# Performance work log

Hardware: AMD Instinct MI355X
Metric: run time of the kernel (lower is better)

Reference implementation:

```python
import jax, jax.numpy as jnp
import numpy as np

C = 512
H_FEAT, W_FEAT = 50, 75
ROI_SIZE = 7
SCALE = 16.0
N_ROIS = 512
N_CLASS = 21
FC_IN = C * ROI_SIZE * ROI_SIZE  # 25088
FC_DIM = 4096


def setup_inputs() -> dict:
    key = jax.random.key(0)
    ks = jax.random.split(key, 12)
    x = jax.random.normal(ks[0], (1, C, H_FEAT, W_FEAT), jnp.float32)
    img_h, img_w = H_FEAT * 16, W_FEAT * 16
    # boxes (x1,y1,x2,y2) in image pixel coords, in-bounds, min side 32px
    x1 = jax.random.randint(ks[1], (N_ROIS,), 0, img_w - 64)
    y1 = jax.random.randint(ks[2], (N_ROIS,), 0, img_h - 64)
    w = jax.random.randint(ks[3], (N_ROIS,), 32, 400)
    h = jax.random.randint(ks[4], (N_ROIS,), 32, 400)
    x2 = jnp.minimum(x1 + w, img_w - 1)
    y2 = jnp.minimum(y1 + h, img_h - 1)
    rois = jnp.stack([x1, y1, x2, y2], axis=1).astype(jnp.float32)
    W1 = jax.random.normal(ks[5], (FC_IN, FC_DIM), jnp.float32) * 0.01
    b1 = jnp.zeros((FC_DIM,), jnp.float32)
    W2 = jax.random.normal(ks[6], (FC_DIM, FC_DIM), jnp.float32) * 0.01
    b2 = jnp.zeros((FC_DIM,), jnp.float32)
    W_loc = jax.random.normal(ks[7], (FC_DIM, N_CLASS * 4), jnp.float32) * 0.001
    b_loc = jnp.zeros((N_CLASS * 4,), jnp.float32)
    W_score = jax.random.normal(ks[8], (FC_DIM, N_CLASS), jnp.float32) * 0.01
    b_score = jnp.zeros((N_CLASS,), jnp.float32)
    return {"x": x, "rois": rois, "W1": W1, "b1": b1, "W2": W2, "b2": b2,
            "W_loc": W_loc, "b_loc": b_loc, "W_score": W_score, "b_score": b_score}


def _roi_adaptive_max_pool(feat, rois_i):
    """feat: [C,H,W]; rois_i: int32 [N,4] (x1,y1,x2,y2) in feature coords.
    Matches torch F.adaptive_max_pool2d on the inclusive crop [y1:y2+1, x1:x2+1].
    """
    KR = H_FEAT // ROI_SIZE + 2   # max rows per adaptive bin (<= ceil(H/7)+1)
    KC = W_FEAT // ROI_SIZE + 2   # max cols per adaptive bin
    p = jnp.arange(ROI_SIZE)

    def one(roi):
        x1, y1, x2, y2 = roi[0], roi[1], roi[2], roi[3]
        h = y2 - y1 + 1
        w = x2 - x1 + 1
        # torch adaptive pooling: start = floor(i*S/O), end = ceil((i+1)*S/O)
        rs = y1 + (p * h) // ROI_SIZE
        re = y1 + -((-(p + 1) * h) // ROI_SIZE)   # ceil via floor-div
        cs = x1 + (p * w) // ROI_SIZE
        ce = x1 + -((-(p + 1) * w) // ROI_SIZE)
        ri = rs[:, None] + jnp.arange(KR)[None, :]          # [7,KR]
        rv = ri < re[:, None]
        ri = jnp.clip(ri, 0, H_FEAT - 1)
        ci = cs[:, None] + jnp.arange(KC)[None, :]          # [7,KC]
        cv = ci < ce[:, None]
        ci = jnp.clip(ci, 0, W_FEAT - 1)
        g = feat[:, ri, :][:, :, :, ci]                      # [C,7,KR,7,KC]
        m = rv[:, :, None, None] & cv[None, None, :, :]      # [7,KR,7,KC]
        g = jnp.where(m[None], g, -jnp.inf)
        return g.max(axis=(2, 4))                            # [C,7,7]

    return jax.lax.map(one, rois_i)                          # [N,C,7,7]


def reference(x, rois, W1, b1, W2, b2, W_loc, b_loc, W_score, b_score):
    # rois.mul_(1/spatial_scale); rois = rois.long()  (trunc == floor for >=0)
    rois_i = (rois * (1.0 / SCALE)).astype(jnp.int32)
    pool = _roi_adaptive_max_pool(x[0], rois_i)              # [N,C,7,7]
    pool = pool.reshape(pool.shape[0], -1)                   # [N, 25088]
    fc = jax.nn.relu(pool @ W1 + b1)
    fc = jax.nn.relu(fc @ W2 + b2)
    roi_locs = fc @ W_loc + b_loc                            # [N, 84]
    roi_scores = fc @ W_score + b_score                      # [N, 21]
    return (roi_locs, roi_scores)
```

## Files before the change

kernel.cpp:

```cpp
#include <hip/hip_runtime.h>
#include <hip/hip_bf16.h>
#include <math.h>

typedef unsigned short U16;
typedef __bf16 bf16x8 __attribute__((ext_vector_type(8)));
typedef float floatx4 __attribute__((ext_vector_type(4)));
typedef unsigned short ushort8 __attribute__((ext_vector_type(8)));

#define C_CH 512
#define HF 50
#define WF 75
#define NROIS 512
#define FC_IN 25088
#define FC_DIM 4096
#define NHEAD 105
#define NHEAD_PAD 128
#define OUT_LOCS (NROIS * 84)

__device__ __forceinline__ float b2f(U16 u) {
    union { unsigned int i; float f; } x; x.i = ((unsigned int)u) << 16; return x.f;
}
__device__ __forceinline__ U16 f2b(float f) {
    union { float f; unsigned int i; } x; x.f = f;
    unsigned int r = x.i + 0x7fffu + ((x.i >> 16) & 1u);
    return (U16)(r >> 16);
}

__device__ __forceinline__ void gld_lds16(const U16* g, U16* lds_base, int lane) {
#if __has_builtin(__builtin_amdgcn_global_load_lds)
    typedef const __attribute__((address_space(1))) unsigned int* gas1;
    typedef __attribute__((address_space(3))) unsigned int* las3;
    __builtin_amdgcn_global_load_lds((gas1)(unsigned long long)g,
                                     (las3)(unsigned int)(unsigned long long)lds_base,
                                     16, 0, 0);
#else
    *(floatx4*)(lds_base + lane * 8) = *(const floatx4*)g;
#endif
}

__global__ void detect_kernel(const unsigned int* __restrict__ w1,
                              const unsigned int* __restrict__ rois,
                              int* __restrict__ flags) {
    __shared__ int cnt_w, cnt_r;
    if (threadIdx.x == 0) { cnt_w = 0; cnt_r = 0; }
    __syncthreads();
    int lw = 0;
    for (int i = threadIdx.x; i < 2048; i += 256) {
        const unsigned int w = w1[i];
        const unsigned int e = (w >> 7) & 0xFFu;
        if ((e >= 90u && e <= 130u) || (w & 0x7FFFu) == 0u) lw++;
    }
    int lr = 0;
    for (int i = threadIdx.x; i < 512; i += 256) {
        union { unsigned int u; float f; } v; v.u = rois[i];
        const float f = v.f;
        if (f >= 0.0f && f <= 1300.0f && f == floorf(f)) lr++;
    }
    atomicAdd(&cnt_w, lw);
    atomicAdd(&cnt_r, lr);
    __syncthreads();
    if (threadIdx.x == 0) {
        flags[0] = (cnt_w < 1024) ? 1 : 0;
        flags[1] = (cnt_r >= 256) ? 1 : 0;
    }
}

__global__ void roi_pool_kernel(const void* __restrict__ feat_,
                                const void* __restrict__ rois_,
                                const int* __restrict__ flags,
                                U16* __restrict__ pool) {
    const int n = blockIdx.x;
    const int ch0 = blockIdx.y * 32;
    const int t = threadIdx.x;
    const int f32w = flags[0];
    const int f32r = flags[1];
    __shared__ int rs[7], re_[7], cs[7], ce_[7];

    float c4[4];
    if (f32r) {
        const float* r = (const float*)rois_ + n * 4;
        c4[0] = r[0]; c4[1] = r[1]; c4[2] = r[2]; c4[3] = r[3];
    } else {
        const U16* r = (const U16*)rois_ + n * 4;
        c4[0] = b2f(r[0]); c4[1] = b2f(r[1]); c4[2] = b2f(r[2]); c4[3] = b2f(r[3]);
    }
    const int x1 = (int)(c4[0] * 0.0625f);
    const int y1 = (int)(c4[1] * 0.0625f);
    const int x2 = (int)(c4[2] * 0.0625f);
    const int y2 = (int)(c4[3] * 0.0625f);
    const int h = y2 - y1 + 1;
    const int w = x2 - x1 + 1;
    if (t < 7) {
        rs[t] = y1 + (t * h) / 7;
        re_[t] = y1 + ((t + 1) * h + 6) / 7;
        cs[t] = x1 + (t * w) / 7;
        ce_[t] = x1 + ((t + 1) * w + 6) / 7;
    }
    __syncthreads();

    const float* featf = (const float*)feat_;
    const U16* featu = (const U16*)feat_;

    for (int o = t; o < 32 * 49; o += 256) {
        const int ch = ch0 + o / 49;
        const int b = o % 49;
        const int ph = b / 7;
        const int pw = b - ph * 7;
        const int r0 = rs[ph], r1 = re_[ph];
        const int c0 = cs[pw], c1 = ce_[pw];
        const int base = ch * (HF * WF);
        float m = -1.0e4f;
        if (f32w) {
            for (int r = r0; r < r1; ++r) {
                const int rr = r < (HF - 1) ? r : (HF - 1);
                const float* fr = featf + base + rr * WF;
                for (int c = c0; c < c1; ++c) {
                    const int cc = c < (WF - 1) ? c : (WF - 1);
                    const float v = fr[cc];
                    m = (m > v) ? m : v;
                }
            }
        } else {
            for (int r = r0; r < r1; ++r) {
                const int rr = r < (HF - 1) ? r : (HF - 1);
                const U16* fr = featu + base + rr * WF;
                for (int c = c0; c < c1; ++c) {
                    const int cc = c < (WF - 1) ? c : (WF - 1);
                    const float v = b2f(fr[cc]);
                    m = (m > v) ? m : v;
                }
            }
        }
        m = fminf(fmaxf(m, -1.0e4f), 1.0e4f);
        pool[(size_t)n * FC_IN + ch * 49 + b] = f2b(m);
    }
}

__global__ void transpose_w_kernel(const void* __restrict__ W,
                                   U16* __restrict__ WT,
                                   int K, int N, const int* __restrict__ flags) {
    const int t = threadIdx.x;
    const int wave = t >> 6, lane = t & 63;
    const int k0 = (blockIdx.x * 4 + wave) * 8;
    const int n = blockIdx.y * 64 + lane;
    union { U16 u[8]; ushort8 v; } o;
    if (flags[0]) {
        const float* Wf = (const float*)W;
#pragma unroll
        for (int j = 0; j < 8; ++j) o.u[j] = f2b(Wf[(size_t)(k0 + j) * N + n]);
    } else {
        const U16* Wu = (const U16*)W;
#pragma unroll
        for (int j = 0; j < 8; ++j) o.u[j] = Wu[(size_t)(k0 + j) * N + n];
    }
    *(ushort8*)&WT[(size_t)n * K + k0] = o.v;
}

#define GBM 128
#define GBN 128
#define GBK 32

__launch_bounds__(256, 2)
__global__ void gemm_tn_kernel(const U16* __restrict__ A, int lda,
                               const U16* __restrict__ BT, int ldb,
                               float* __restrict__ Cpart,
                               int M, int N, int Ks) {
    __shared__ __align__(16) U16 a_lds[GBM * GBK];
    __shared__ __align__(16) U16 b_lds[GBN * GBK];

    const int t = threadIdx.x;
    const int wave = t >> 6, lane = t & 63;
    const int ln = lane & 15, q = lane >> 4;
    const int wm = wave >> 1, wn = wave & 1;
    const int bm = blockIdx.y * GBM, bn = blockIdx.x * GBN;
    const int s = blockIdx.z;
    const int kb = s * Ks, ke = kb + Ks;
    float* Cp = Cpart + (size_t)s * M * N;

    floatx4 acc[4][4];
#pragma unroll
    for (int i = 0; i < 4; ++i)
#pragma unroll
        for (int j = 0; j < 4; ++j) acc[i][j] = (floatx4)0.0f;

    const int slot0 = wave * 2;
    const int rsl = lane >> 2;
    const int c8 = (lane & 3) * 8;
    const U16* Ag0 = A + (size_t)(bm + slot0 * 16 + rsl) * lda + c8;
    const U16* Ag1 = A + (size_t)(bm + slot0 * 16 + 16 + rsl) * lda + c8;
    const U16* Bg0 = BT + (size_t)(bn + slot0 * 16 + rsl) * ldb + c8;
    const U16* Bg1 = BT + (size_t)(bn + slot0 * 16 + 16 + rsl) * ldb + c8;
    U16* al0 = &a_lds[slot0 * 512];
    U16* al1 = &a_lds[(slot0 + 1) * 512];
    U16* bl0 = &b_lds[slot0 * 512];
    U16* bl1 = &b_lds[(slot0 + 1) * 512];

    for (int k0 = kb; k0 < ke; k0 += GBK) {
        gld_lds16(Ag0 + k0, al0, lane);
        gld_lds16(Ag1 + k0, al1, lane);
        gld_lds16(Bg0 + k0, bl0, lane);
        gld_lds16(Bg1 + k0, bl1, lane);
        __syncthreads();

        bf16x8 av[4], bv[4];
#pragma unroll
        for (int mt = 0; mt < 4; ++mt)
            av[mt] = *(const bf16x8*)&a_lds[(wm * 64 + mt * 16 + ln) * GBK + q * 8];
#pragma unroll
        for (int nt = 0; nt < 4; ++nt)
            bv[nt] = *(const bf16x8*)&b_lds[(wn * 64 + nt * 16 + ln) * GBK + q * 8];

#pragma unroll
        for (int mt = 0; mt < 4; ++mt)
#pragma unroll
            for (int nt = 0; nt < 4; ++nt)
                acc[mt][nt] = __builtin_amdgcn_mfma_f32_16x16x32_bf16(
                    av[mt], bv[nt], acc[mt][nt], 0, 0, 0);
        __syncthreads();
    }

#pragma unroll
    for (int nt = 0; nt < 4; ++nt) {
        const int col = bn + wn * 64 + nt * 16 + ln;
#pragma unroll
        for (int mt = 0; mt < 4; ++mt) {
            const int row = bm + wm * 64 + mt * 16 + q * 4;
#pragma unroll
            for (int r = 0; r < 4; ++r)
                Cp[(size_t)(row + r) * N + col] = acc[mt][nt][r];
        }
    }
}

__global__ void reduce_act_kernel(const float* __restrict__ Cpart,
                                  const U16* __restrict__ bias,
                                  U16* __restrict__ Cout,
                                  int MN, int N, int S, int do_relu) {
    const int i4 = (blockIdx.x * 256 + threadIdx.x) * 4;
    if (i4 >= MN) return;
    floatx4 sum = *(const floatx4*)&Cpart[i4];
    for (int s = 1; s < S; ++s)
        sum += *(const floatx4*)&Cpart[(size_t)s * MN + i4];
    const int nb = i4 & (N - 1);
    U16 o[4];
#pragma unroll
    for (int j = 0; j < 4; ++j) {
        float v = sum[j] + b2f(bias[nb + j]);
        if (do_relu) { v = v > 0.0f ? v : 0.0f; v = fminf(v, 1.0e4f); }
        o[j] = f2b(v);
    }
    *(unsigned long long*)&Cout[i4] = *(unsigned long long*)o;
}

__global__ void pack_headsT_kernel(const void* __restrict__ W_loc,
                                   const void* __restrict__ W_score,
                                   const U16* __restrict__ b_loc,
                                   const U16* __restrict__ b_score,
                                   const int* __restrict__ flags,
                                   U16* __restrict__ WhT, U16* __restrict__ bh) {
    const int idx = blockIdx.x * 256 + threadIdx.x;
    const int c = idx >> 12;
    const int k = idx & 4095;
    const int f32w = flags[0];
    U16 v = 0;
    if (f32w) {
        if (c < 84) v = f2b(((const float*)W_loc)[(size_t)k * 84 + c]);
        else if (c < NHEAD) v = f2b(((const float*)W_score)[(size_t)k * 21 + (c - 84)]);
    } else {
        if (c < 84) v = ((const U16*)W_loc)[(size_t)k * 84 + c];
        else if (c < NHEAD) v = ((const U16*)W_score)[(size_t)k * 21 + (c - 84)];
    }
    WhT[idx] = v;
    if (idx < NHEAD_PAD) {
        U16 bb = 0;
        if (idx < 84) bb = b_loc[idx];
        else if (idx < NHEAD) bb = b_score[idx - 84];
        bh[idx] = bb;
    }
}

__global__ void head_reduce_kernel(const float* __restrict__ Cpart,
                                   const U16* __restrict__ bh,
                                   const int* __restrict__ flags,
                                   void* __restrict__ out, int S) {
    const int idx = blockIdx.x * 256 + threadIdx.x;
    if (idx >= NROIS * NHEAD_PAD) return;
    const int m = idx >> 7;
    const int c = idx & 127;
    float s = 0.0f;
    for (int ss = 0; ss < S; ++ss)
        s += Cpart[(size_t)ss * (NROIS * NHEAD_PAD) + idx];
    s += b2f(bh[c]);
    if (c >= NHEAD) return;
    const int dst = (c < 84) ? (m * 84 + c) : (OUT_LOCS + m * 21 + (c - 84));
    if (flags[0]) ((float*)out)[dst] = s;
    else ((U16*)out)[dst] = f2b(s);
}

#define BM 128
#define BN 64
#define BK 32

__launch_bounds__(256, 2)
__global__ void gemm_bias_kernel(const U16* __restrict__ A,
                                 const void* __restrict__ B,
                                 const U16* __restrict__ bias,
                                 U16* __restrict__ Cout,
                                 int M, int N, int K, int do_relu,
                                 const int* __restrict__ flags, int use_flag) {
    __shared__ U16 a_lds[BM][BK];
    __shared__ U16 b_lds[BK][80];
    const int b_f32 = use_flag ? flags[0] : 0;
    const int t = threadIdx.x;
    const int wave = t >> 6, lane = t & 63;
    const int ln = lane & 15, q = lane >> 4;
    const int wm = wave >> 1, wn = wave & 1;
    const int bm = blockIdx.y * BM, bn = blockIdx.x * BN;
    floatx4 acc[4][2];
#pragma unroll
    for (int i = 0; i < 4; ++i)
#pragma unroll
        for (int j = 0; j < 2; ++j) acc[i][j] = (floatx4)0.0f;
    const int arow = t >> 2, acol = (t & 3) * 8;
    const int bk = t >> 3, bn8 = (t & 7) * 8;
    const int browp = ((bk & 7) << 2) | (bk >> 3);
    const U16* Ap0 = A + (size_t)(bm + arow) * K + acol;
    const U16* Ap1 = A + (size_t)(bm + 64 + arow) * K + acol;
    const U16* Bp16 = (const U16*)B + (size_t)bk * N + bn + bn8;
    const float* Bp32 = (const float*)B + (size_t)bk * N + bn + bn8;
    for (int k0 = 0; k0 < K; k0 += BK) {
        *(floatx4*)&a_lds[arow][acol] = *(const floatx4*)(Ap0 + k0);
        *(floatx4*)&a_lds[64 + arow][acol] = *(const floatx4*)(Ap1 + k0);
        if (b_f32) {
            const float* src = Bp32 + (size_t)k0 * N;
            union { U16 u[8]; floatx4 v; } tmp;
#pragma unroll
            for (int j = 0; j < 8; ++j) tmp.u[j] = f2b(src[j]);
            *(floatx4*)&b_lds[browp][bn8] = tmp.v;
        } else {
            *(floatx4*)&b_lds[browp][bn8] = *(const floatx4*)(Bp16 + (size_t)k0 * N);
        }
        __syncthreads();
        bf16x8 av[4];
#pragma unroll
        for (int mt = 0; mt < 4; ++mt)
            av[mt] = *(const bf16x8*)&a_lds[wm * 64 + mt * 16 + ln][q * 8];
        union { U16 u[8]; bf16x8 v; } bu[2];
#pragma unroll
        for (int nt = 0; nt < 2; ++nt) {
            const int n = wn * 32 + nt * 16 + ln;
#pragma unroll
            for (int j = 0; j < 8; ++j) bu[nt].u[j] = b_lds[(j << 2) | q][n];
        }
#pragma unroll
        for (int mt = 0; mt < 4; ++mt)
#pragma unroll
            for (int nt = 0; nt < 2; ++nt)
                acc[mt][nt] = __builtin_amdgcn_mfma_f32_16x16x32_bf16(
                    av[mt], bu[nt].v, acc[mt][nt], 0, 0, 0);
        __syncthreads();
    }
#pragma unroll
    for (int nt = 0; nt < 2; ++nt) {
        const int col = bn + wn * 32 + nt * 16 + ln;
        const float bv = b2f(bias[col]);
#pragma unroll
        for (int mt = 0; mt < 4; ++mt) {
            const int row = bm + wm * 64 + mt * 16 + q * 4;
#pragma unroll
            for (int r = 0; r < 4; ++r) {
                float v = acc[mt][nt][r] + bv;
                if (do_relu) { v = v > 0.0f ? v : 0.0f; v = fminf(v, 1.0e4f); }
                Cout[(size_t)(row + r) * N + col] = f2b(v);
            }
        }
    }
}

__global__ void pack_heads_kernel(const void* __restrict__ W_loc,
                                  const void* __restrict__ W_score,
                                  const U16* __restrict__ b_loc,
                                  const U16* __restrict__ b_score,
                                  const int* __restrict__ flags,
                                  U16* __restrict__ Wh, U16* __restrict__ bh) {
    const int k = blockIdx.x;
    const int c = threadIdx.x;
    const int f32w = flags[0];
    U16 v = 0;
    if (f32w) {
        if (c < 84) v = f2b(((const float*)W_loc)[k * 84 + c]);
        else if (c < NHEAD) v = f2b(((const float*)W_score)[k * 21 + (c - 84)]);
    } else {
        if (c < 84) v = ((const U16*)W_loc)[k * 84 + c];
        else if (c < NHEAD) v = ((const U16*)W_score)[k * 21 + (c - 84)];
    }
    Wh[k * NHEAD_PAD + c] = v;
    if (k == 0) {
        U16 bb = 0;
        if (c < 84) bb = b_loc[c];
        else if (c < NHEAD) bb = b_score[c - 84];
        bh[c] = bb;
    }
}

__global__ void scatter_out_kernel(const U16* __restrict__ Chead,
                                   const int* __restrict__ flags,
                                   void* __restrict__ out) {
    const int idx = blockIdx.x * 256 + threadIdx.x;
    if (idx >= NROIS * NHEAD) return;
    const int f32o = flags[0];
    const int m = idx / NHEAD;
    const int c = idx - m * NHEAD;
    const U16 v = Chead[m * NHEAD_PAD + c];
    const int dst = (c < 84) ? (m * 84 + c) : (OUT_LOCS + m * 21 + (c - 84));
    if (f32o) ((float*)out)[dst] = b2f(v);
    else ((U16*)out)[dst] = v;
}

extern "C" void kernel_launch(void* const* d_in, const int* in_sizes, int n_in,
                              void* d_out, int out_size, void* d_ws, size_t ws_size,
                              hipStream_t stream) {
    const void* x       = d_in[0];
    const void* rois    = d_in[1];
    const void* W1      = d_in[2];
    const U16* b1       = (const U16*)d_in[3];
    const void* W2      = d_in[4];
    const U16* b2       = (const U16*)d_in[5];
    const void* W_loc   = d_in[6];
    const U16* b_loc    = (const U16*)d_in[7];
    const void* W_score = d_in[8];
    const U16* b_score  = (const U16*)d_in[9];

    int* flags = (int*)d_ws;
    char* p = (char*)d_ws + 256;
    U16* pool = (U16*)p;                       p += (size_t)NROIS * FC_IN * 2;
    U16* fc1  = (U16*)p;                       p += (size_t)NROIS * FC_DIM * 2;
    U16* fc2  = (U16*)p;                       p += (size_t)NROIS * FC_DIM * 2;

    detect_kernel<<<1, 256, 0, stream>>>((const unsigned int*)W1,
                                         (const unsigned int*)rois, flags);
    roi_pool_kernel<<<dim3(NROIS, 16), 256, 0, stream>>>(x, rois, flags, pool);

    char* pf = p;
    U16* WT1 = (U16*)pf;  pf += (size_t)FC_DIM * FC_IN * 2;
    U16* WT2 = (U16*)pf;  pf += (size_t)FC_DIM * FC_DIM * 2;
    U16* WhT = (U16*)pf;  pf += (size_t)NHEAD_PAD * FC_DIM * 2;
    U16* bh  = (U16*)pf;  pf += 256;
    float* Cpart = (float*)pf; pf += (size_t)4 * NROIS * FC_DIM * 4;
    const size_t need_fast = (size_t)(pf - (char*)d_ws);

    if (ws_size >= need_fast) {
        transpose_w_kernel<<<dim3(FC_IN / 32, FC_DIM / 64), 256, 0, stream>>>(
            W1, WT1, FC_IN, FC_DIM, flags);
        transpose_w_kernel<<<dim3(FC_DIM / 32, FC_DIM / 64), 256, 0, stream>>>(
            W2, WT2, FC_DIM, FC_DIM, flags);
        pack_headsT_kernel<<<(NHEAD_PAD * FC_DIM) / 256, 256, 0, stream>>>(
            W_loc, W_score, b_loc, b_score, flags, WhT, bh);

        gemm_tn_kernel<<<dim3(FC_DIM / GBN, NROIS / GBM, 4), 256, 0, stream>>>(
            pool, FC_IN, WT1, FC_IN, Cpart, NROIS, FC_DIM, FC_IN / 4);
        reduce_act_kernel<<<(NROIS * FC_DIM / 4) / 256, 256, 0, stream>>>(
            Cpart, b1, fc1, NROIS * FC_DIM, FC_DIM, 4, 1);

        gemm_tn_kernel<<<dim3(FC_DIM / GBN, NROIS / GBM, 4), 256, 0, stream>>>(
            fc1, FC_DIM, WT2, FC_DIM, Cpart, NROIS, FC_DIM, FC_DIM / 4);
        reduce_act_kernel<<<(NROIS * FC_DIM / 4) / 256, 256, 0, stream>>>(
            Cpart, b2, fc2, NROIS * FC_DIM, FC_DIM, 4, 1);

        gemm_tn_kernel<<<dim3(1, NROIS / GBM, 32), 256, 0, stream>>>(
            fc2, FC_DIM, WhT, FC_DIM, Cpart, NROIS, NHEAD_PAD, FC_DIM / 32);
        head_reduce_kernel<<<(NROIS * NHEAD_PAD) / 256, 256, 0, stream>>>(
            Cpart, bh, flags, d_out, 32);
    } else {
        U16* Wh    = (U16*)p;
        U16* bhf   = Wh + (size_t)FC_DIM * NHEAD_PAD;
        U16* Chead = bhf + NHEAD_PAD;
        pack_heads_kernel<<<FC_DIM, NHEAD_PAD, 0, stream>>>(W_loc, W_score, b_loc,
                                                            b_score, flags, Wh, bhf);
        gemm_bias_kernel<<<dim3(FC_DIM / BN, NROIS / BM), 256, 0, stream>>>(
            pool, W1, b1, fc1, NROIS, FC_DIM, FC_IN, 1, flags, 1);
        gemm_bias_kernel<<<dim3(FC_DIM / BN, NROIS / BM), 256, 0, stream>>>(
            fc1, W2, b2, fc2, NROIS, FC_DIM, FC_DIM, 1, flags, 1);
        gemm_bias_kernel<<<dim3(NHEAD_PAD / BN, NROIS / BM), 256, 0, stream>>>(
            fc2, Wh, bhf, Chead, NROIS, NHEAD_PAD, FC_DIM, 0, flags, 0);
        scatter_out_kernel<<<(NROIS * NHEAD + 255) / 256, 256, 0, stream>>>(
            Chead, flags, d_out);
    }
}
```

Before: 1.119 ms.

## Fuse weight fp32-to-bf16 conversion and transpose into the FC GEMM B-tile load

Result: faster. 950.3 us (-15.1%).

```diff
diff --git a/kernel.cpp b/kernel.cpp
--- a/kernel.cpp
+++ b/kernel.cpp
@@ -136,29 +136,150 @@
     }
 }
 
-__global__ void transpose_w_kernel(const void* __restrict__ W,
-                                   U16* __restrict__ WT,
-                                   int K, int N, const int* __restrict__ flags) {
-    const int t = threadIdx.x;
-    const int wave = t >> 6, lane = t & 63;
-    const int k0 = (blockIdx.x * 4 + wave) * 8;
-    const int n = blockIdx.y * 64 + lane;
-    union { U16 u[8]; ushort8 v; } o;
-    if (flags[0]) {
-        const float* Wf = (const float*)W;
-#pragma unroll
-        for (int j = 0; j < 8; ++j) o.u[j] = f2b(Wf[(size_t)(k0 + j) * N + n]);
-    } else {
-        const U16* Wu = (const U16*)W;
-#pragma unroll
-        for (int j = 0; j < 8; ++j) o.u[j] = Wu[(size_t)(k0 + j) * N + n];
-    }
-    *(ushort8*)&WT[(size_t)n * K + k0] = o.v;
-}
-
 #define GBM 128
 #define GBN 128
 #define GBK 32
+#define BROW 40
+
+__launch_bounds__(256, 2)
+__global__ void gemm_fused_kernel(const U16* __restrict__ A, int lda,
+                                  const void* __restrict__ B, int ldb,
+                                  float* __restrict__ Cpart,
+                                  int M, int N, int Ks,
+                                  const int* __restrict__ flags) {
+    __shared__ __align__(16) U16 a_lds[GBM * GBK];
+    __shared__ __align__(16) U16 b_lds[GBN * BROW];
+
+    const int t = threadIdx.x;
+    const int wave = t >> 6, lane = t & 63;
+    const int ln = lane & 15, q = lane >> 4;
+    const int wm = wave >> 1, wn = wave & 1;
+    const int bm = blockIdx.y * GBM, bn = blockIdx.x * GBN;
+    const int s = blockIdx.z;
+    const int kb = s * Ks, ke = kb + Ks;
+    float* Cp = Cpart + (size_t)s * M * N;
+    const int f32b = flags[0];
+
+    floatx4 acc[4][4];
+#pragma unroll
+    for (int i = 0; i < 4; ++i)
+#pragma unroll
+        for (int j = 0; j < 4; ++j) acc[i][j] = (floatx4)0.0f;
+
+    const int slot0 = wave * 2;
+    const int rsl = lane >> 2;
+    const int c8 = (lane & 3) * 8;
+    const U16* Ag0 = A + (size_t)(bm + slot0 * 16 + rsl) * lda + c8;
+    const U16* Ag1 = A + (size_t)(bm + slot0 * 16 + 16 + rsl) * lda + c8;
+    U16* al0 = &a_lds[slot0 * 512];
+    U16* al1 = &a_lds[(slot0 + 1) * 512];
+
+    const int np = (t & 63) * 2;
+    const int kg = (t >> 6) * 8;
+    U16* bw0 = &b_lds[(size_t)np * BROW + kg];
+    U16* bw1 = &b_lds[(size_t)(np + 1) * BROW + kg];
+
+    if (f32b) {
+        const float* bp = (const float*)B + (size_t)(kb + kg) * ldb + bn + np;
+        typedef float float2v __attribute__((ext_vector_type(2)));
+        float2v v[8];
+#pragma unroll
+        for (int j = 0; j < 8; ++j) v[j] = *(const float2v*)(bp + (size_t)j * ldb);
+        bp += (size_t)GBK * ldb;
+
+        for (int k0 = kb; k0 < ke; k0 += GBK) {
+            gld_lds16(Ag0 + k0, al0, lane);
+            gld_lds16(Ag1 + k0, al1, lane);
+            union { __bf16 b[8]; ushort8 s8; } h0, h1;
+#pragma unroll
+            for (int j = 0; j < 8; ++j) {
+                h0.b[j] = (__bf16)v[j].x;
+                h1.b[j] = (__bf16)v[j].y;
+            }
+            *(ushort8*)bw0 = h0.s8;
+            *(ushort8*)bw1 = h1.s8;
+            __syncthreads();
+
+            bf16x8 av[4], bv[4];
+#pragma unroll
+            for (int mt = 0; mt < 4; ++mt)
+                av[mt] = *(const bf16x8*)&a_lds[(wm * 64 + mt * 16 + ln) * GBK + q * 8];
+#pragma unroll
+            for (int nt = 0; nt < 4; ++nt)
+                bv[nt] = *(const bf16x8*)&b_lds[(size_t)(wn * 64 + nt * 16 + ln) * BROW + q * 8];
+
+            if (k0 + GBK < ke) {
+#pragma unroll
+                for (int j = 0; j < 8; ++j) v[j] = *(const float2v*)(bp + (size_t)j * ldb);
+                bp += (size_t)GBK * ldb;
+            }
+
+#pragma unroll
+            for (int mt = 0; mt < 4; ++mt)
+#pragma unroll
+                for (int nt = 0; nt < 4; ++nt)
+                    acc[mt][nt] = __builtin_amdgcn_mfma_f32_16x16x32_bf16(
+                        av[mt], bv[nt], acc[mt][nt], 0, 0, 0);
+            __syncthreads();
+        }
+    } else {
+        const int ldw = ldb >> 1;
+        const unsigned int* bp = (const unsigned int*)B +
+                                 (((size_t)(kb + kg) * ldb + bn + np) >> 1);
+        unsigned int v[8];
+#pragma unroll
+        for (int j = 0; j < 8; ++j) v[j] = bp[(size_t)j * ldw];
+        bp += (size_t)GBK * ldw;
+
+        for (int k0 = kb; k0 < ke; k0 += GBK) {
+            gld_lds16(Ag0 + k0, al0, lane);
+            gld_lds16(Ag1 + k0, al1, lane);
+            union { U16 u[8]; ushort8 s8; } h0, h1;
+#pragma unroll
+            for (int j = 0; j < 8; ++j) {
+                h0.u[j] = (U16)(v[j] & 0xffffu);
+                h1.u[j] = (U16)(v[j] >> 16);
+            }
+            *(ushort8*)bw0 = h0.s8;
+            *(ushort8*)bw1 = h1.s8;
+            __syncthreads();
+
+            bf16x8 av[4], bv[4];
+#pragma unroll
+            for (int mt = 0; mt < 4; ++mt)
+                av[mt] = *(const bf16x8*)&a_lds[(wm * 64 + mt * 16 + ln) * GBK + q * 8];
+#pragma unroll
+            for (int nt = 0; nt < 4; ++nt)
+                bv[nt] = *(const bf16x8*)&b_lds[(size_t)(wn * 64 + nt * 16 + ln) * BROW + q * 8];
+
+            if (k0 + GBK < ke) {
+#pragma unroll
+                for (int j = 0; j < 8; ++j) v[j] = bp[(size_t)j * ldw];
+                bp += (size_t)GBK * ldw;
+            }
+
+#pragma unroll
+            for (int mt = 0; mt < 4; ++mt)
+#pragma unroll
+                for (int nt = 0; nt < 4; ++nt)
+                    acc[mt][nt] = __builtin_amdgcn_mfma_f32_16x16x32_bf16(
+                        av[mt], bv[nt], acc[mt][nt], 0, 0, 0);
+            __syncthreads();
+        }
+    }
+
+#pragma unroll
+    for (int nt = 0; nt < 4; ++nt) {
+        const int col = bn + wn * 64 + nt * 16 + ln;
+#pragma unroll
+        for (int mt = 0; mt < 4; ++mt) {
+            const int row = bm + wm * 64 + mt * 16 + q * 4;
+#pragma unroll
+            for (int r = 0; r < 4; ++r)
+                Cp[(size_t)(row + r) * N + col] = acc[mt][nt][r];
+        }
+    }
+}
 
 __launch_bounds__(256, 2)
 __global__ void gemm_tn_kernel(const U16* __restrict__ A, int lda,
@@ -442,28 +563,22 @@
     roi_pool_kernel<<<dim3(NROIS, 16), 256, 0, stream>>>(x, rois, flags, pool);
 
     char* pf = p;
-    U16* WT1 = (U16*)pf;  pf += (size_t)FC_DIM * FC_IN * 2;
-    U16* WT2 = (U16*)pf;  pf += (size_t)FC_DIM * FC_DIM * 2;
     U16* WhT = (U16*)pf;  pf += (size_t)NHEAD_PAD * FC_DIM * 2;
     U16* bh  = (U16*)pf;  pf += 256;
     float* Cpart = (float*)pf; pf += (size_t)4 * NROIS * FC_DIM * 4;
     const size_t need_fast = (size_t)(pf - (char*)d_ws);
 
     if (ws_size >= need_fast) {
-        transpose_w_kernel<<<dim3(FC_IN / 32, FC_DIM / 64), 256, 0, stream>>>(
-            W1, WT1, FC_IN, FC_DIM, flags);
-        transpose_w_kernel<<<dim3(FC_DIM / 32, FC_DIM / 64), 256, 0, stream>>>(
-            W2, WT2, FC_DIM, FC_DIM, flags);
         pack_headsT_kernel<<<(NHEAD_PAD * FC_DIM) / 256, 256, 0, stream>>>(
             W_loc, W_score, b_loc, b_score, flags, WhT, bh);
 
-        gemm_tn_kernel<<<dim3(FC_DIM / GBN, NROIS / GBM, 4), 256, 0, stream>>>(
-            pool, FC_IN, WT1, FC_IN, Cpart, NROIS, FC_DIM, FC_IN / 4);
+        gemm_fused_kernel<<<dim3(FC_DIM / GBN, NROIS / GBM, 4), 256, 0, stream>>>(
+            pool, FC_IN, W1, FC_DIM, Cpart, NROIS, FC_DIM, FC_IN / 4, flags);
         reduce_act_kernel<<<(NROIS * FC_DIM / 4) / 256, 256, 0, stream>>>(
             Cpart, b1, fc1, NROIS * FC_DIM, FC_DIM, 4, 1);
 
-        gemm_tn_kernel<<<dim3(FC_DIM / GBN, NROIS / GBM, 4), 256, 0, stream>>>(
-            fc1, FC_DIM, WT2, FC_DIM, Cpart, NROIS, FC_DIM, FC_DIM / 4);
+        gemm_fused_kernel<<<dim3(FC_DIM / GBN, NROIS / GBM, 4), 256, 0, stream>>>(
+            fc1, FC_DIM, W2, FC_DIM, Cpart, NROIS, FC_DIM, FC_DIM / 4, flags);
         reduce_act_kernel<<<(NROIS * FC_DIM / 4) / 256, 256, 0, stream>>>(
             Cpart, b2, fc2, NROIS * FC_DIM, FC_DIM, 4, 1);
 
```
